# Kernel optimization log

Measured on AMD Instinct MI355X. Metric: run time of the kernel, lower is better.

The kernel has to match this reference:

```python
import jax, jax.numpy as jnp
import numpy as np

# ultralytics ops.non_max_suppression defaults
CONF_THRES = 0.25
IOU_THRES = 0.45
MAX_DET = 300          # max detections returned per image
MAX_WH = 7680.0        # class-offset constant for class-aware NMS
MAX_NMS = 1024         # fixed candidate cap (ultralytics uses 30000; fixed-size for jit)


def _xywh2xyxy(x):
    # x: [..., 4] (cx, cy, w, h) -> (x1, y1, x2, y2)
    xy, half_wh = x[..., :2], x[..., 2:] * 0.5
    return jnp.concatenate([xy - half_wh, xy + half_wh], axis=-1)


def _pairwise_iou(b):
    # b: [K, 4] xyxy -> [K, K] IoU
    area = (b[:, 2] - b[:, 0]) * (b[:, 3] - b[:, 1])
    lt = jnp.maximum(b[:, None, :2], b[None, :, :2])
    rb = jnp.minimum(b[:, None, 2:], b[None, :, 2:])
    wh = jnp.clip(rb - lt, 0.0)
    inter = wh[..., 0] * wh[..., 1]
    return inter / (area[:, None] + area[None, :] - inter + 1e-7)


def _nms_single(pred):
    # pred: [4+nc, N] raw detector output for one image
    boxes = _xywh2xyxy(pred[:4].T)          # [N, 4]
    scores = pred[4:].T                     # [N, nc]
    conf = scores.max(axis=-1)              # [N]
    cls = scores.argmax(axis=-1).astype(pred.dtype)  # [N]

    valid = conf > CONF_THRES
    masked_conf = jnp.where(valid, conf, -1.0)
    top_conf, idx = jax.lax.top_k(masked_conf, MAX_NMS)   # sorted desc
    b = boxes[idx]                          # [K, 4]
    c = cls[idx]                            # [K]

    # class-aware NMS via coordinate offset per class
    iou = _pairwise_iou(b + c[:, None] * MAX_WH)          # [K, K]

    keep0 = top_conf > CONF_THRES
    ar = jnp.arange(MAX_NMS)

    def body(i, keep):
        # greedy: if box i is kept, suppress all lower-scored boxes with high IoU
        sup = keep[i] & (iou[i] > IOU_THRES) & (ar > i)
        return keep & ~sup

    keep = jax.lax.fori_loop(0, MAX_NMS, body, keep0)

    kept_conf = jnp.where(keep, top_conf, -1.0)
    det_conf, di = jax.lax.top_k(kept_conf, MAX_DET)
    det = jnp.concatenate(
        [b[di], det_conf[:, None], c[di][:, None]], axis=-1)  # [MAX_DET, 6]
    ok = (det_conf > CONF_THRES)[:, None]
    return jnp.where(ok, det, 0.0)


def setup_inputs() -> dict:
    key = jax.random.key(0)
    # [batch, 4+nc, num_anchors]: xywh in [0,1), class scores in [0,1)
    preds = jax.random.uniform(key, (32, 84, 8400), dtype=jnp.float32)
    return {"preds": preds}


def reference(preds):
    dets = jax.vmap(_nms_single)(preds)  # [B, MAX_DET, 6] (xyxy, conf, cls)
    return dets[0]                       # module returns preds[0]
```

## Files before the change

kernel.cpp:

```cpp
#include <hip/hip_runtime.h>
#include <cstdint>
#include <cstddef>


#define NA    8400
#define NCLS  80
#define NTOP  1024
#define NDET  300
#define CONF_T 0.25f
#define IOU_T  0.45f
#define MAXWH  7680.0f

#define NSLICE 25
#define SLICEW 336

#define OFF_KEY   0
#define OFF_CLS   33600
#define OFF_CONF  67200
#define OFF_SCONF 100800
#define OFF_SX1   104896
#define OFF_SY1   108992
#define OFF_SX2   113088
#define OFF_SY2   117184
#define OFF_SCLS  121280
#define OFF_SUP   125376
#define OFF_RANK  256448

typedef unsigned long long u64;
typedef unsigned int u32;

__device__ __forceinline__ int sw(int j) { return j + (j >> 6); }

__device__ __forceinline__ u32 f2mono(float f) {
    u32 u = __float_as_uint(f);
    return u ^ ((u & 0x80000000u) ? 0xFFFFFFFFu : 0x80000000u);
}
__device__ __forceinline__ float mono2f(u32 m) {
    u32 u = (m & 0x80000000u) ? (m ^ 0x80000000u) : ~m;
    return __uint_as_float(u);
}
__device__ __forceinline__ u64 rl64(u64 v, int g) {
    u32 lo = (u32)__builtin_amdgcn_readlane((int)(u32)v, g);
    u32 hi = (u32)__builtin_amdgcn_readlane((int)(u32)(v >> 32), g);
    return ((u64)hi << 32) | lo;
}

__global__ __launch_bounds__(1024) void k_confcls(const float* __restrict__ pred,
                                                  u32* __restrict__ key,
                                                  float* __restrict__ clsf,
                                                  float* __restrict__ conf,
                                                  u32* __restrict__ rank)
{
    __shared__ u64 pk[8][128];
    int tid = threadIdx.x;
    int q = tid >> 7, t = tid & 127;
    int a = blockIdx.x * 128 + t;
    u64 pv = 0ULL;
    if (a < NA) {
        const float* s = pred + (size_t)(4 + q * 10) * NA;
        float best = s[a];
        int bc = q * 10;
#pragma unroll
        for (int c = 1; c < 10; ++c) {
            float v = s[(size_t)c * NA + a];
            if (v > best) { best = v; bc = q * 10 + c; }
        }
        pv = ((u64)f2mono(best) << 32) | (u32)(255 - bc);
    }
    pk[q][t] = pv;
    __syncthreads();
    if (q == 0 && a < NA) {
        u64 mm = pk[0][t];
#pragma unroll
        for (int r = 1; r < 8; ++r) { u64 v = pk[r][t]; if (v > mm) mm = v; }
        float best = mono2f((u32)(mm >> 32));
        int bc = 255 - (int)(mm & 0xFFu);
        float m = (best > CONF_T) ? best : -1.0f;
        key[a]  = ~f2mono(m);
        clsf[a] = (float)bc;
        conf[a] = m;
        rank[a] = 0u;
    }
}

__global__ __launch_bounds__(256) void k_rank_partial(const u32* __restrict__ key,
                                                      u32* __restrict__ rank)
{
    __shared__ __align__(16) u32 kh[SLICEW];
    int tid = threadIdx.x;
    int s   = blockIdx.y;
    int jb  = s * SLICEW;
    for (int k = tid; k < SLICEW; k += 256) kh[k] = key[jb + k];
    __syncthreads();

    int a = blockIdx.x * 256 + tid;
    if (a >= NA) return;

    u64 myk = (((u64)key[a]) << 32) | (u32)a;
    u32 r = 0;
    const uint4* kv4 = (const uint4*)kh;
#pragma unroll 4
    for (int j4 = 0; j4 < SLICEW / 4; ++j4) {
        uint4 kk = kv4[j4];
        u32 j = (u32)jb + (u32)j4 * 4u;
        r += ((((u64)kk.x) << 32) | (j + 0u)) < myk;
        r += ((((u64)kk.y) << 32) | (j + 1u)) < myk;
        r += ((((u64)kk.z) << 32) | (j + 2u)) < myk;
        r += ((((u64)kk.w) << 32) | (j + 3u)) < myk;
    }
    atomicAdd(&rank[a], r);
}

__global__ __launch_bounds__(256) void k_scatter(const float* __restrict__ pred,
                                                 const u32* __restrict__ rank,
                                                 const float* __restrict__ clsf,
                                                 const float* __restrict__ conf,
                                                 float* __restrict__ wsf)
{
    int a = blockIdx.x * 256 + threadIdx.x;
    if (a >= NA) return;
    u32 r = rank[a];
    if (r < NTOP) {
#pragma clang fp contract(off)
        float x = pred[0 * NA + a], y = pred[1 * NA + a];
        float w = pred[2 * NA + a], h = pred[3 * NA + a];
        float hw = w * 0.5f, hh = h * 0.5f;
        wsf[OFF_SCONF / 4 + r] = conf[a];
        wsf[OFF_SX1  / 4 + r] = x - hw;
        wsf[OFF_SY1  / 4 + r] = y - hh;
        wsf[OFF_SX2  / 4 + r] = x + hw;
        wsf[OFF_SY2  / 4 + r] = y + hh;
        wsf[OFF_SCLS / 4 + r] = clsf[a];
    }
}

__global__ __launch_bounds__(128) void k_supmat(const float* __restrict__ wsf,
                                                u64* __restrict__ sup)
{
#pragma clang fp contract(off)
    __shared__ float4 obox[NTOP + 16];
    __shared__ float  oar[NTOP + 16];
    int tid = threadIdx.x;
    for (int k = tid; k < NTOP; k += 128) {
        float cls = wsf[OFF_SCLS / 4 + k];
        float off = cls * MAXWH;
        float x1 = wsf[OFF_SX1 / 4 + k] + off;
        float y1 = wsf[OFF_SY1 / 4 + k] + off;
        float x2 = wsf[OFF_SX2 / 4 + k] + off;
        float y2 = wsf[OFF_SY2 / 4 + k] + off;
        int si = sw(k);
        obox[si] = make_float4(x1, y1, x2, y2);
        oar[si]  = (x2 - x1) * (y2 - y1);
    }
    __syncthreads();

    int gid = blockIdx.x * 128 + tid;
    int i = gid >> 4;
    int l = gid & 15;
    int si = sw(i);
    float4 bb = obox[si];
    float  ba = oar[si];
    u64 bits = 0ULL;
    int j0 = l << 6;
#pragma unroll 4
    for (int jj = 0; jj < 64; ++jj) {
        int j = j0 + jj;
        int sj = sw(j);
        float4 ob = obox[sj];
        float xx1 = fmaxf(bb.x, ob.x);
        float yy1 = fmaxf(bb.y, ob.y);
        float xx2 = fminf(bb.z, ob.z);
        float yy2 = fminf(bb.w, ob.w);
        float w  = fmaxf(xx2 - xx1, 0.0f);
        float hh = fmaxf(yy2 - yy1, 0.0f);
        float inter = w * hh;
        float denom = ba + oar[sj] - inter + 1e-7f;
        bool s = (j > i) && ((inter / denom) > IOU_T);
        bits |= ((u64)s) << jj;
    }
    sup[(size_t)i * 16 + l] = bits;
}

__global__ __launch_bounds__(256) void k_nms_out(const float* __restrict__ wsf,
                                                 const u64* __restrict__ sup,
                                                 float* __restrict__ out)
{
    __shared__ u64 lsup[NTOP * 16];
    __shared__ u64 tg[16 * 64];
    __shared__ u64 lkeep[64];
    __shared__ u64 kc[16];
    __shared__ u32 pcs[16];
    int tid  = threadIdx.x;
    int lane = tid & 63;
    int wv   = tid >> 6;

    {
        const uint4* gs = (const uint4*)sup;
        uint4* lv = (uint4*)lsup;
        for (int idx = tid; idx < NTOP * 8; idx += 256) {
            uint4 v = gs[idx];
            lv[idx] = v;
            int row = idx >> 3;
            int c   = (idx & 7) * 2;
            int g   = row >> 6;
            if (c == g)     tg[(g << 6) + (row & 63)] = (((u64)v.y) << 32) | v.x;
            if (c + 1 == g) tg[(g << 6) + (row & 63)] = (((u64)v.w) << 32) | v.z;
        }
    }

    const float* sconf = wsf + OFF_SCONF / 4;
    for (int base = 0; base < NTOP; base += 256) {
        u64 b = __ballot(sconf[base + tid] > CONF_T);
        if (lane == 0) kc[(base >> 6) + wv] = b;
    }
    __syncthreads();

    if (wv == 0) {
        int l   = lane & 15;
        int rep = lane >> 4;
        u64 keep = kc[l];
        for (int g = 0; g < 16; ++g) {
            u64 scur = rl64(keep, g) & rl64(keep, 16 + g) &
                       rl64(keep, 32 + g) & rl64(keep, 48 + g);
            u64 rgv = tg[(g << 6) + lane];
#pragma unroll
            for (int ii = 0; ii < 64; ++ii) {
                u64 rg  = rl64(rgv, ii);
                u64 sel = 0ULL - ((scur >> ii) & 1ULL);
                scur &= ~(rg & sel);
            }
#pragma unroll 4
            for (int b = 0; b < 16; ++b) {
                int i_loc = (b << 2) + rep;
                u64 rl = lsup[(((g << 6) + i_loc) << 4) + l];
                u64 m  = 0ULL - ((scur >> i_loc) & 1ULL);
                keep &= ~(rl & m);
            }
        }
        lkeep[lane] = keep;
    }
    __syncthreads();

    if (tid < 16) {
        u64 kk = lkeep[tid] & lkeep[16 + tid] & lkeep[32 + tid] & lkeep[48 + tid];
        kc[tid]  = kk;
        pcs[tid] = (u32)__popcll(kk);
    }
    __syncthreads();

    for (int r = tid; r < NDET; r += 256) {
        int acc = 0, chunk = -1, off = 0;
#pragma unroll
        for (int c = 0; c < 16; ++c) {
            int p = (int)pcs[c];
            if (chunk < 0 && r < acc + p) { chunk = c; off = r - acc; }
            acc += p;
        }
        float o0 = 0.f, o1 = 0.f, o2 = 0.f, o3 = 0.f, o4 = 0.f, o5 = 0.f;
        if (chunk >= 0) {
            u64 mk = kc[chunk];
            for (int q = 0; q < off; ++q) mk &= mk - 1ULL;
            int p = chunk * 64 + __builtin_ctzll(mk);
            o0 = wsf[OFF_SX1  / 4 + p];
            o1 = wsf[OFF_SY1  / 4 + p];
            o2 = wsf[OFF_SX2  / 4 + p];
            o3 = wsf[OFF_SY2  / 4 + p];
            o4 = wsf[OFF_SCONF / 4 + p];
            o5 = wsf[OFF_SCLS / 4 + p];
        }
        out[r * 6 + 0] = o0; out[r * 6 + 1] = o1; out[r * 6 + 2] = o2;
        out[r * 6 + 3] = o3; out[r * 6 + 4] = o4; out[r * 6 + 5] = o5;
    }
}

extern "C" void kernel_launch(void* const* d_in, const int* in_sizes, int n_in,
                              void* d_out, int out_size, void* d_ws, size_t ws_size,
                              hipStream_t stream)
{
    const float* preds = (const float*)d_in[0];
    char* ws = (char*)d_ws;
    u32* key    = (u32*)(ws + OFF_KEY);
    float* clsf = (float*)(ws + OFF_CLS);
    float* conf = (float*)(ws + OFF_CONF);
    float* wsf  = (float*)ws;
    u64* sup    = (u64*)(ws + OFF_SUP);
    u32* rank   = (u32*)(ws + OFF_RANK);
    float* out  = (float*)d_out;

    hipLaunchKernelGGL(k_confcls,      dim3(66),         dim3(1024), 0, stream, preds, key, clsf, conf, rank);
    hipLaunchKernelGGL(k_rank_partial, dim3(33, NSLICE), dim3(256),  0, stream, key, rank);
    hipLaunchKernelGGL(k_scatter,      dim3(33),         dim3(256),  0, stream, preds, rank, clsf, conf, wsf);
    hipLaunchKernelGGL(k_supmat,       dim3(128),        dim3(128),  0, stream, wsf, sup);
    hipLaunchKernelGGL(k_nms_out,      dim3(1),          dim3(256),  0, stream, wsf, sup, out);
}
```

Before: 183.2 us.

## Fuse NMS pipeline into one cooperative kernel with grid syncs

Replaces five separate kernel launches with a single cooperative kernel of 256 blocks that uses grid.sync() between the stages: confidence/class, ranking, suppression-matrix construction and the final NMS. The ranking stage now stages all 8400 keys in LDS and each anchor's rank is reduced across eight lanes with shuffles instead of global atomics. The suppression matrix is split over four lanes per word, and the class-max reduction also uses shuffles. This is meant to remove launch gaps and intermediate global round-trips. In exchange it relies on cooperative-launch residency and uses about 136 KB of LDS per block, which may limit occupancy.

```diff
diff --git a/kernel.cpp b/kernel.cpp
--- a/kernel.cpp
+++ b/kernel.cpp
@@ -1,35 +1,29 @@
 #include <hip/hip_runtime.h>
+#include <hip/hip_cooperative_groups.h>
 #include <cstdint>
 #include <cstddef>
 
+namespace cg = cooperative_groups;
+
 
 #define NA    8400
-#define NCLS  80
 #define NTOP  1024
 #define NDET  300
 #define CONF_T 0.25f
 #define IOU_T  0.45f
 #define MAXWH  7680.0f
 
-#define NSLICE 25
-#define SLICEW 336
-
 #define OFF_KEY   0
-#define OFF_CLS   33600
-#define OFF_CONF  67200
-#define OFF_SCONF 100800
-#define OFF_SX1   104896
-#define OFF_SY1   108992
-#define OFF_SX2   113088
-#define OFF_SY2   117184
-#define OFF_SCLS  121280
-#define OFF_SUP   125376
-#define OFF_RANK  256448
+#define OFF_SCONF 33600
+#define OFF_SX1   37696
+#define OFF_SY1   41792
+#define OFF_SX2   45888
+#define OFF_SY2   49984
+#define OFF_SCLS  54080
+#define OFF_SUP   58176
 
 typedef unsigned long long u64;
 typedef unsigned int u32;
-
-__device__ __forceinline__ int sw(int j) { return j + (j >> 6); }
 
 __device__ __forceinline__ u32 f2mono(float f) {
     u32 u = __float_as_uint(f);
@@ -44,232 +38,221 @@
     u32 hi = (u32)__builtin_amdgcn_readlane((int)(u32)(v >> 32), g);
     return ((u64)hi << 32) | lo;
 }
-
-__global__ __launch_bounds__(1024) void k_confcls(const float* __restrict__ pred,
-                                                  u32* __restrict__ key,
-                                                  float* __restrict__ clsf,
-                                                  float* __restrict__ conf,
-                                                  u32* __restrict__ rank)
-{
-    __shared__ u64 pk[8][128];
-    int tid = threadIdx.x;
-    int q = tid >> 7, t = tid & 127;
-    int a = blockIdx.x * 128 + t;
-    u64 pv = 0ULL;
-    if (a < NA) {
-        const float* s = pred + (size_t)(4 + q * 10) * NA;
-        float best = s[a];
-        int bc = q * 10;
-#pragma unroll
-        for (int c = 1; c < 10; ++c) {
-            float v = s[(size_t)c * NA + a];
-            if (v > best) { best = v; bc = q * 10 + c; }
-        }
-        pv = ((u64)f2mono(best) << 32) | (u32)(255 - bc);
-    }
-    pk[q][t] = pv;
-    __syncthreads();
-    if (q == 0 && a < NA) {
-        u64 mm = pk[0][t];
-#pragma unroll
-        for (int r = 1; r < 8; ++r) { u64 v = pk[r][t]; if (v > mm) mm = v; }
-        float best = mono2f((u32)(mm >> 32));
-        int bc = 255 - (int)(mm & 0xFFu);
-        float m = (best > CONF_T) ? best : -1.0f;
-        key[a]  = ~f2mono(m);
-        clsf[a] = (float)bc;
-        conf[a] = m;
-        rank[a] = 0u;
-    }
-}
-
-__global__ __launch_bounds__(256) void k_rank_partial(const u32* __restrict__ key,
-                                                      u32* __restrict__ rank)
-{
-    __shared__ __align__(16) u32 kh[SLICEW];
-    int tid = threadIdx.x;
-    int s   = blockIdx.y;
-    int jb  = s * SLICEW;
-    for (int k = tid; k < SLICEW; k += 256) kh[k] = key[jb + k];
-    __syncthreads();
-
-    int a = blockIdx.x * 256 + tid;
-    if (a >= NA) return;
-
-    u64 myk = (((u64)key[a]) << 32) | (u32)a;
+__device__ __forceinline__ u64 sx64(u64 v, int m) {
+    return (u64)__shfl_xor((long long)v, m, 64);
+}
+__device__ __forceinline__ int swc(int j) { return j + (j >> 4); }
+
+__device__ __forceinline__ void conf_one(const float* __restrict__ pred, int a, int q,
+                                         u32* __restrict__ key, float& mout, int& bcout) {
+    const float* s = pred + (size_t)(4 + q * 10) * NA;
+    float best = s[a];
+    int bc = q * 10;
+#pragma unroll
+    for (int c = 1; c < 10; ++c) {
+        float v = s[(size_t)c * NA + a];
+        if (v > best) { best = v; bc = q * 10 + c; }
+    }
+    u64 pv = ((u64)f2mono(best) << 32) | (u32)(255 - bc);
+    u64 x;
+    x = sx64(pv, 1); if (x > pv) pv = x;
+    x = sx64(pv, 2); if (x > pv) pv = x;
+    x = sx64(pv, 4); if (x > pv) pv = x;
+    if (q == 0) {
+        float bst = mono2f((u32)(pv >> 32));
+        int bcw = 255 - (int)(pv & 0xFFu);
+        float m = (bst > CONF_T) ? bst : -1.0f;
+        key[a] = ~f2mono(m);
+        mout = m; bcout = bcw;
+    }
+}
+
+__device__ __forceinline__ void rank_one(const u32* __restrict__ skeys,
+                                         const float* __restrict__ pred,
+                                         float* __restrict__ wsf,
+                                         int a, int q, float m, int bc) {
+    u64 myk = (((u64)skeys[a]) << 32) | (u32)a;
     u32 r = 0;
-    const uint4* kv4 = (const uint4*)kh;
+    const uint4* kv4 = (const uint4*)skeys;
 #pragma unroll 4
-    for (int j4 = 0; j4 < SLICEW / 4; ++j4) {
-        uint4 kk = kv4[j4];
-        u32 j = (u32)jb + (u32)j4 * 4u;
+    for (int i4 = q; i4 < NA / 4; i4 += 8) {
+        uint4 kk = kv4[i4];
+        u32 j = (u32)i4 * 4u;
         r += ((((u64)kk.x) << 32) | (j + 0u)) < myk;
         r += ((((u64)kk.y) << 32) | (j + 1u)) < myk;
         r += ((((u64)kk.z) << 32) | (j + 2u)) < myk;
         r += ((((u64)kk.w) << 32) | (j + 3u)) < myk;
     }
-    atomicAdd(&rank[a], r);
-}
-
-__global__ __launch_bounds__(256) void k_scatter(const float* __restrict__ pred,
-                                                 const u32* __restrict__ rank,
-                                                 const float* __restrict__ clsf,
-                                                 const float* __restrict__ conf,
-                                                 float* __restrict__ wsf)
-{
-    int a = blockIdx.x * 256 + threadIdx.x;
-    if (a >= NA) return;
-    u32 r = rank[a];
-    if (r < NTOP) {
+    r += (u32)__shfl_xor((int)r, 1);
+    r += (u32)__shfl_xor((int)r, 2);
+    r += (u32)__shfl_xor((int)r, 4);
+    if (q == 0 && r < NTOP) {
 #pragma clang fp contract(off)
-        float x = pred[0 * NA + a], y = pred[1 * NA + a];
-        float w = pred[2 * NA + a], h = pred[3 * NA + a];
+        float x = pred[a], y = pred[NA + a], w = pred[2 * NA + a], h = pred[3 * NA + a];
         float hw = w * 0.5f, hh = h * 0.5f;
-        wsf[OFF_SCONF / 4 + r] = conf[a];
+        wsf[OFF_SCONF / 4 + r] = m;
         wsf[OFF_SX1  / 4 + r] = x - hw;
         wsf[OFF_SY1  / 4 + r] = y - hh;
         wsf[OFF_SX2  / 4 + r] = x + hw;
         wsf[OFF_SY2  / 4 + r] = y + hh;
-        wsf[OFF_SCLS / 4 + r] = clsf[a];
-    }
-}
-
-__global__ __launch_bounds__(128) void k_supmat(const float* __restrict__ wsf,
-                                                u64* __restrict__ sup)
+        wsf[OFF_SCLS / 4 + r] = (float)bc;
+    }
+}
+
+__global__ __launch_bounds__(256) void k_all(const float* __restrict__ pred,
+                                             u32* __restrict__ key,
+                                             float* __restrict__ wsf,
+                                             u64* __restrict__ sup,
+                                             float* __restrict__ out)
 {
-#pragma clang fp contract(off)
-    __shared__ float4 obox[NTOP + 16];
-    __shared__ float  oar[NTOP + 16];
-    int tid = threadIdx.x;
-    for (int k = tid; k < NTOP; k += 128) {
-        float cls = wsf[OFF_SCLS / 4 + k];
-        float off = cls * MAXWH;
-        float x1 = wsf[OFF_SX1 / 4 + k] + off;
-        float y1 = wsf[OFF_SY1 / 4 + k] + off;
-        float x2 = wsf[OFF_SX2 / 4 + k] + off;
-        float y2 = wsf[OFF_SY2 / 4 + k] + off;
-        int si = sw(k);
-        obox[si] = make_float4(x1, y1, x2, y2);
-        oar[si]  = (x2 - x1) * (y2 - y1);
-    }
-    __syncthreads();
-
-    int gid = blockIdx.x * 128 + tid;
-    int i = gid >> 4;
-    int l = gid & 15;
-    int si = sw(i);
-    float4 bb = obox[si];
-    float  ba = oar[si];
-    u64 bits = 0ULL;
-    int j0 = l << 6;
-#pragma unroll 4
-    for (int jj = 0; jj < 64; ++jj) {
-        int j = j0 + jj;
-        int sj = sw(j);
-        float4 ob = obox[sj];
-        float xx1 = fmaxf(bb.x, ob.x);
-        float yy1 = fmaxf(bb.y, ob.y);
-        float xx2 = fminf(bb.z, ob.z);
-        float yy2 = fminf(bb.w, ob.w);
-        float w  = fmaxf(xx2 - xx1, 0.0f);
-        float hh = fmaxf(yy2 - yy1, 0.0f);
-        float inter = w * hh;
-        float denom = ba + oar[sj] - inter + 1e-7f;
-        bool s = (j > i) && ((inter / denom) > IOU_T);
-        bits |= ((u64)s) << jj;
-    }
-    sup[(size_t)i * 16 + l] = bits;
-}
-
-__global__ __launch_bounds__(256) void k_nms_out(const float* __restrict__ wsf,
-                                                 const u64* __restrict__ sup,
-                                                 float* __restrict__ out)
-{
-    __shared__ u64 lsup[NTOP * 16];
-    __shared__ u64 tg[16 * 64];
+    __shared__ __align__(16) char shbuf[139264];
+    u32*    skeys = (u32*)shbuf;
+    float4* obox  = (float4*)shbuf;
+    float*  oar   = (float*)(shbuf + 17408);
+    u64*    lsup  = (u64*)shbuf;
+    u64*    tgb   = (u64*)(shbuf + 131072);
     __shared__ u64 lkeep[64];
     __shared__ u64 kc[16];
     __shared__ u32 pcs[16];
-    int tid  = threadIdx.x;
-    int lane = tid & 63;
-    int wv   = tid >> 6;
+
+    cg::grid_group grid = cg::this_grid();
+    int t = threadIdx.x;
+    int b = blockIdx.x;
+    int u = b * 256 + t;
+
+    float mA = -1.0f, mT = -1.0f;
+    int bcA = 0, bcT = 0;
+    conf_one(pred, u >> 3, u & 7, key, mA, bcA);
+    if (u < 1664) conf_one(pred, 8192 + (u >> 3), u & 7, key, mT, bcT);
+    grid.sync();
 
     {
+        const uint4* kg = (const uint4*)key;
+        uint4* kl = (uint4*)skeys;
+        for (int idx = t; idx < NA / 4; idx += 256) kl[idx] = kg[idx];
+        __syncthreads();
+        rank_one(skeys, pred, wsf, u >> 3, u & 7, mA, bcA);
+        if (u < 1664) rank_one(skeys, pred, wsf, 8192 + (u >> 3), u & 7, mT, bcT);
+    }
+    grid.sync();
+
+    {
+#pragma clang fp contract(off)
+        for (int k = t; k < NTOP; k += 256) {
+            float cls = wsf[OFF_SCLS / 4 + k];
+            float off = cls * MAXWH;
+            float x1 = wsf[OFF_SX1 / 4 + k] + off;
+            float y1 = wsf[OFF_SY1 / 4 + k] + off;
+            float x2 = wsf[OFF_SX2 / 4 + k] + off;
+            float y2 = wsf[OFF_SY2 / 4 + k] + off;
+            int si = swc(k);
+            obox[si] = make_float4(x1, y1, x2, y2);
+            oar[si]  = (x2 - x1) * (y2 - y1);
+        }
+        __syncthreads();
+        int i = u >> 6, l = (u >> 2) & 15, s = u & 3;
+        float4 bb = obox[swc(i)];
+        float  ba = oar[swc(i)];
+        u64 bits = 0ULL;
+        int j0 = (l << 6) + (s << 4);
+#pragma unroll
+        for (int jj = 0; jj < 16; ++jj) {
+            int j = j0 + jj;
+            int sj = swc(j);
+            float4 ob = obox[sj];
+            float xx1 = fmaxf(bb.x, ob.x);
+            float yy1 = fmaxf(bb.y, ob.y);
+            float xx2 = fminf(bb.z, ob.z);
+            float yy2 = fminf(bb.w, ob.w);
+            float w  = fmaxf(xx2 - xx1, 0.0f);
+            float hh = fmaxf(yy2 - yy1, 0.0f);
+            float inter = w * hh;
+            float denom = ba + oar[sj] - inter + 1e-7f;
+            bool fl = (j > i) && ((inter / denom) > IOU_T);
+            bits |= ((u64)fl) << ((s << 4) + jj);
+        }
+        bits |= sx64(bits, 1);
+        bits |= sx64(bits, 2);
+        if (s == 0) sup[(size_t)i * 16 + l] = bits;
+    }
+    grid.sync();
+
+    if (b == 0) {
         const uint4* gs = (const uint4*)sup;
         uint4* lv = (uint4*)lsup;
-        for (int idx = tid; idx < NTOP * 8; idx += 256) {
+        for (int idx = t; idx < NTOP * 8; idx += 256) {
             uint4 v = gs[idx];
             lv[idx] = v;
             int row = idx >> 3;
             int c   = (idx & 7) * 2;
             int g   = row >> 6;
-            if (c == g)     tg[(g << 6) + (row & 63)] = (((u64)v.y) << 32) | v.x;
-            if (c + 1 == g) tg[(g << 6) + (row & 63)] = (((u64)v.w) << 32) | v.z;
-        }
-    }
-
-    const float* sconf = wsf + OFF_SCONF / 4;
-    for (int base = 0; base < NTOP; base += 256) {
-        u64 b = __ballot(sconf[base + tid] > CONF_T);
-        if (lane == 0) kc[(base >> 6) + wv] = b;
-    }
-    __syncthreads();
-
-    if (wv == 0) {
-        int l   = lane & 15;
-        int rep = lane >> 4;
-        u64 keep = kc[l];
-        for (int g = 0; g < 16; ++g) {
-            u64 scur = rl64(keep, g) & rl64(keep, 16 + g) &
-                       rl64(keep, 32 + g) & rl64(keep, 48 + g);
-            u64 rgv = tg[(g << 6) + lane];
-#pragma unroll
-            for (int ii = 0; ii < 64; ++ii) {
-                u64 rg  = rl64(rgv, ii);
-                u64 sel = 0ULL - ((scur >> ii) & 1ULL);
-                scur &= ~(rg & sel);
+            if (c == g)     tgb[(g << 6) + (row & 63)] = (((u64)v.y) << 32) | v.x;
+            if (c + 1 == g) tgb[(g << 6) + (row & 63)] = (((u64)v.w) << 32) | v.z;
+        }
+        const float* sconf = wsf + OFF_SCONF / 4;
+        int lane = t & 63, wv = t >> 6;
+        for (int base = 0; base < NTOP; base += 256) {
+            u64 bl = __ballot(sconf[base + t] > CONF_T);
+            if (lane == 0) kc[(base >> 6) + wv] = bl;
+        }
+        __syncthreads();
+
+        if (wv == 0) {
+            int l   = lane & 15;
+            int rep = lane >> 4;
+            u64 keep = kc[l];
+            for (int g = 0; g < 16; ++g) {
+                u64 scur = rl64(keep, g) & rl64(keep, 16 + g) &
+                           rl64(keep, 32 + g) & rl64(keep, 48 + g);
+                u64 rgv = tgb[(g << 6) + lane];
+#pragma unroll
+                for (int ii = 0; ii < 64; ++ii) {
+                    u64 rg  = rl64(rgv, ii);
+                    u64 sel = 0ULL - ((scur >> ii) & 1ULL);
+                    scur &= ~(rg & sel);
+                }
+#pragma unroll 4
+                for (int bb2 = 0; bb2 < 16; ++bb2) {
+                    int i_loc = (bb2 << 2) + rep;
+                    u64 rl = lsup[(((g << 6) + i_loc) << 4) + l];
+                    u64 mm = 0ULL - ((scur >> i_loc) & 1ULL);
+                    keep &= ~(rl & mm);
+                }
             }
-#pragma unroll 4
-            for (int b = 0; b < 16; ++b) {
-                int i_loc = (b << 2) + rep;
-                u64 rl = lsup[(((g << 6) + i_loc) << 4) + l];
-                u64 m  = 0ULL - ((scur >> i_loc) & 1ULL);
-                keep &= ~(rl & m);
+            lkeep[lane] = keep;
+        }
+        __syncthreads();
+
+        if (t < 16) {
+            u64 kk = lkeep[t] & lkeep[16 + t] & lkeep[32 + t] & lkeep[48 + t];
+            kc[t]  = kk;
+            pcs[t] = (u32)__popcll(kk);
+        }
+        __syncthreads();
+
+        for (int r = t; r < NDET; r += 256) {
+            int acc = 0, chunk = -1, off = 0;
+#pragma unroll
+            for (int c = 0; c < 16; ++c) {
+                int p = (int)pcs[c];
+                if (chunk < 0 && r < acc + p) { chunk = c; off = r - acc; }
+                acc += p;
             }
-        }
-        lkeep[lane] = keep;
-    }
-    __syncthreads();
-
-    if (tid < 16) {
-        u64 kk = lkeep[tid] & lkeep[16 + tid] & lkeep[32 + tid] & lkeep[48 + tid];
-        kc[tid]  = kk;
-        pcs[tid] = (u32)__popcll(kk);
-    }
-    __syncthreads();
-
-    for (int r = tid; r < NDET; r += 256) {
-        int acc = 0, chunk = -1, off = 0;
-#pragma unroll
-        for (int c = 0; c < 16; ++c) {
-            int p = (int)pcs[c];
-            if (chunk < 0 && r < acc + p) { chunk = c; off = r - acc; }
-            acc += p;
-        }
-        float o0 = 0.f, o1 = 0.f, o2 = 0.f, o3 = 0.f, o4 = 0.f, o5 = 0.f;
-        if (chunk >= 0) {
-            u64 mk = kc[chunk];
-            for (int q = 0; q < off; ++q) mk &= mk - 1ULL;
-            int p = chunk * 64 + __builtin_ctzll(mk);
-            o0 = wsf[OFF_SX1  / 4 + p];
-            o1 = wsf[OFF_SY1  / 4 + p];
-            o2 = wsf[OFF_SX2  / 4 + p];
-            o3 = wsf[OFF_SY2  / 4 + p];
-            o4 = wsf[OFF_SCONF / 4 + p];
-            o5 = wsf[OFF_SCLS / 4 + p];
-        }
-        out[r * 6 + 0] = o0; out[r * 6 + 1] = o1; out[r * 6 + 2] = o2;
-        out[r * 6 + 3] = o3; out[r * 6 + 4] = o4; out[r * 6 + 5] = o5;
+            float o0 = 0.f, o1 = 0.f, o2 = 0.f, o3 = 0.f, o4 = 0.f, o5 = 0.f;
+            if (chunk >= 0) {
+                u64 mk = kc[chunk];
+                for (int q = 0; q < off; ++q) mk &= mk - 1ULL;
+                int p = chunk * 64 + __builtin_ctzll(mk);
+                o0 = wsf[OFF_SX1  / 4 + p];
+                o1 = wsf[OFF_SY1  / 4 + p];
+                o2 = wsf[OFF_SX2  / 4 + p];
+                o3 = wsf[OFF_SY2  / 4 + p];
+                o4 = wsf[OFF_SCONF / 4 + p];
+                o5 = wsf[OFF_SCLS / 4 + p];
+            }
+            out[r * 6 + 0] = o0; out[r * 6 + 1] = o1; out[r * 6 + 2] = o2;
+            out[r * 6 + 3] = o3; out[r * 6 + 4] = o4; out[r * 6 + 5] = o5;
+        }
     }
 }
 
@@ -279,17 +262,11 @@
 {
     const float* preds = (const float*)d_in[0];
     char* ws = (char*)d_ws;
-    u32* key    = (u32*)(ws + OFF_KEY);
-    float* clsf = (float*)(ws + OFF_CLS);
-    float* conf = (float*)(ws + OFF_CONF);
-    float* wsf  = (float*)ws;
-    u64* sup    = (u64*)(ws + OFF_SUP);
-    u32* rank   = (u32*)(ws + OFF_RANK);
-    float* out  = (float*)d_out;
-
-    hipLaunchKernelGGL(k_confcls,      dim3(66),         dim3(1024), 0, stream, preds, key, clsf, conf, rank);
-    hipLaunchKernelGGL(k_rank_partial, dim3(33, NSLICE), dim3(256),  0, stream, key, rank);
-    hipLaunchKernelGGL(k_scatter,      dim3(33),         dim3(256),  0, stream, preds, rank, clsf, conf, wsf);
-    hipLaunchKernelGGL(k_supmat,       dim3(128),        dim3(128),  0, stream, wsf, sup);
-    hipLaunchKernelGGL(k_nms_out,      dim3(1),          dim3(256),  0, stream, wsf, sup, out);
-}
+    u32*   key = (u32*)(ws + OFF_KEY);
+    float* wsf = (float*)ws;
+    u64*   sup = (u64*)(ws + OFF_SUP);
+    float* out = (float*)d_out;
+
+    void* args[] = { (void*)&preds, (void*)&key, (void*)&wsf, (void*)&sup, (void*)&out };
+    hipLaunchCooperativeKernel((void*)k_all, dim3(256), dim3(256), args, 0, stream);
+}
```

Result: slower. 261.0 us (+42.5%).
